# Kernel tuning notes

Hardware: AMD Instinct MI355X
Metric: run time of the kernel (lower is better)

The kernel has to match this reference:

```python
import jax, jax.numpy as jnp
import numpy as np

K_NEIGHBORS = 3  # init kwarg k_neighbors


def setup_inputs() -> dict:
    key = jax.random.key(0)
    k1, k2 = jax.random.split(key)
    q = jax.random.normal(k1, (75, 640, 21, 21), dtype=jnp.float32)
    S = jax.random.normal(k2, (5, 640, 21, 21), dtype=jnp.float32)
    return {"q": q, "S": S, "qAV_num": 1, "SAV_num": 1, "shot_num": 1}


def reference(q, S, qAV_num, SAV_num, shot_num):
    B, C = q.shape[0], q.shape[1]
    # [B, HW, C], L2-normalize each local descriptor over channels
    qd = q.reshape(B, C, -1).transpose(0, 2, 1)
    qd = qd / jnp.linalg.norm(qd, axis=2, keepdims=True)

    N = S.shape[0]
    sd = S.reshape(N, C, -1).transpose(0, 2, 1)  # [N, HW, C]
    sd = sd / jnp.linalg.norm(sd, axis=2, keepdims=True)
    HW = sd.shape[1]
    M = SAV_num * shot_num * HW
    # group support images into classes: [ncls, C, M]
    sup = sd.reshape(-1, M, C).transpose(0, 2, 1)
    ncls = sup.shape[0]

    # cosine similarity: [B, ncls, HW, M]
    ip = jnp.einsum('bqc,ncm->bnqm', qd, sup)
    # split AV groups: [B//qAV, qAV, ncls, HW, M]
    ip = ip.reshape(B // qAV_num, qAV_num, ncls, HW, M)
    # top-k along the query-descriptor (HW) axis (torch dim=-2)
    topk = jax.lax.top_k(jnp.swapaxes(ip, -1, -2), K_NEIGHBORS)[0]  # [..., M, k]
    img2class = topk.sum(axis=(-1, -2))  # [B', qAV, ncls]
    # geometric mean over the AV axis (dim=1)
    sim = jnp.exp(jnp.mean(jnp.log(img2class), axis=1))  # [B', ncls]
    return sim
```

## Files before the change

### kernel.cpp

```cpp
#include <hip/hip_runtime.h>
#include <hip/hip_bf16.h>


#define B_IMGS 75
#define N_CLS  5
#define C_DIM  640
#define HW     441
#define HWP    448
#define NKT    20
#define NRB    28
#define CHUNK  512

typedef __attribute__((ext_vector_type(8))) short  short8;
typedef __attribute__((ext_vector_type(4))) float  float4v;

__device__ __forceinline__ void ins3(float& t0, float& t1, float& t2, float v) {
    float m  = fminf(t0, v);
    t0 = fmaxf(t0, v);
    float m2 = fminf(t1, m);
    t1 = fmaxf(t1, m);
    t2 = fmaxf(t2, m2);
}

__device__ __forceinline__ void glds16(const __hip_bfloat16* g, __hip_bfloat16* l) {
    __builtin_amdgcn_global_load_lds(
        (const __attribute__((address_space(1))) unsigned int*)g,
        (__attribute__((address_space(3))) unsigned int*)l, 16, 0, 0);
}

__global__ __launch_bounds__(256)
void prep_kernel(const float* __restrict__ q, const float* __restrict__ S,
                 __hip_bfloat16* __restrict__ qn2, __hip_bfloat16* __restrict__ sn2) {
    __shared__ __hip_bfloat16 tile[C_DIM][65];
    __shared__ float part[4][64];
    __shared__ float inv[64];

    int bid = blockIdx.x;
    int img = bid / 7;
    int h0  = bid % 7;
    const float* src; __hip_bfloat16* dst;
    if (img < B_IMGS) {
        src = q + (size_t)img * C_DIM * HW;
        dst = qn2 + (size_t)img * NRB * NKT * CHUNK;
    } else {
        src = S + (size_t)(img - B_IMGS) * C_DIM * HW;
        dst = sn2 + (size_t)(img - B_IMGS) * NRB * NKT * CHUNK;
    }
    int t  = threadIdx.x;
    int hl = t & 63;
    int p  = t >> 6;
    int hw = h0 * 64 + hl;
    bool ok = hw < HW;
    int hwc = ok ? hw : (HW - 1);

    float ss = 0.f;
#pragma unroll 16
    for (int c = p * 160; c < (p + 1) * 160; ++c) {
        float v = src[(size_t)c * HW + hwc];
        ss += v * v;
    }
    part[p][hl] = ss;
    __syncthreads();
    if (t < 64) {
        float tot = part[0][t] + part[1][t] + part[2][t] + part[3][t];
        bool okr = (h0 * 64 + t) < HW;
        inv[t] = okr ? rsqrtf(tot) : 0.f;
    }
    __syncthreads();

    float iv = inv[hl];
#pragma unroll 8
    for (int c = p * 160; c < (p + 1) * 160; ++c) {
        float v = src[(size_t)c * HW + hwc] * iv;
        tile[c][hl] = __float2bfloat16(v);
    }
    __syncthreads();

    int rl  = t >> 2;
    int k8  = (t & 3) * 8;
    int rb  = h0 * 4 + (rl >> 4);
    int r16 = rl & 15;
    for (int kt = 0; kt < NKT; ++kt) {
        short8 v;
#pragma unroll
        for (int j = 0; j < 8; ++j) {
            __hip_bfloat16 h = tile[kt * 32 + k8 + j][rl];
            v[j] = *(short*)&h;
        }
        *(short8*)(dst + ((size_t)rb * NKT + kt) * CHUNK + r16 * 32 + k8) = v;
    }
}

__global__ __launch_bounds__(256, 2)
void gemm_top3_kernel(const __hip_bfloat16* __restrict__ qn2,
                      const __hip_bfloat16* __restrict__ sn2,
                      float* __restrict__ out) {
    __shared__ __hip_bfloat16 sbuf[64 * CHUNK];
    __shared__ float mrg[4][64][3];

    int id  = blockIdx.x;
    int xcd = id & 7;
    int j8  = id >> 3;
    int b   = (j8 / 35) * 8 + xcd;
    if (b >= B_IMGS) return;
    int inner = j8 % 35;
    int n  = inner / 7;
    int mt = inner % 7;

    int tid  = threadIdx.x;
    int w    = tid >> 6;
    int lane = tid & 63;
    int c16  = lane & 15;
    int quad = lane >> 4;
    int frag = c16 * 32 + quad * 8;

    const __hip_bfloat16* qA = qn2 + (size_t)b * NRB * NKT * CHUNK;
    const __hip_bfloat16* qB = sn2 + ((size_t)n * NRB + mt * 4) * NKT * CHUNK;

    float4v acc[7][4];
#pragma unroll
    for (int r = 0; r < 7; ++r)
#pragma unroll
        for (int j = 0; j < 4; ++j)
            acc[r][j] = (float4v){0.f, 0.f, 0.f, 0.f};

    for (int s = 0; s < 10; ++s) {
        __syncthreads();
#pragma unroll
        for (int i = 0; i < 16; ++i) {
            int cid = w * 16 + i;
            const __hip_bfloat16* g;
            if (cid < 56) {
                int rb = cid >> 1;
                g = qA + ((size_t)rb * NKT + 2 * s + (cid & 1)) * CHUNK;
            } else {
                int jb = (cid - 56) >> 1;
                g = qB + ((size_t)jb * NKT + 2 * s + (cid & 1)) * CHUNK;
            }
            glds16(g + lane * 8, sbuf + cid * CHUNK + lane * 8);
        }
        __syncthreads();

#pragma unroll
        for (int kk = 0; kk < 2; ++kk) {
            short8 a[7], bfr[4];
#pragma unroll
            for (int r = 0; r < 7; ++r)
                a[r] = *(const short8*)(sbuf + ((r * 4 + w) * 2 + kk) * CHUNK + frag);
#pragma unroll
            for (int j = 0; j < 4; ++j)
                bfr[j] = *(const short8*)(sbuf + (56 + j * 2 + kk) * CHUNK + frag);
#pragma unroll
            for (int r = 0; r < 7; ++r)
#pragma unroll
                for (int j = 0; j < 4; ++j)
                    acc[r][j] = __builtin_amdgcn_mfma_f32_16x16x32_bf16(
                        a[r], bfr[j], acc[r][j], 0, 0, 0);
        }
    }

    float T0[4], T1[4], T2[4];
#pragma unroll
    for (int j = 0; j < 4; ++j) { T0[j] = -1e30f; T1[j] = -1e30f; T2[j] = -1e30f; }
#pragma unroll
    for (int r = 0; r < 7; ++r)
#pragma unroll
        for (int j = 0; j < 4; ++j)
#pragma unroll
            for (int g = 0; g < 4; ++g) {
                int row = r * 64 + w * 16 + quad * 4 + g;
                float v = (row < HW) ? acc[r][j][g] : -1e30f;
                ins3(T0[j], T1[j], T2[j], v);
            }

#pragma unroll
    for (int j = 0; j < 4; ++j) {
#pragma unroll
        for (int d = 16; d <= 32; d <<= 1) {
            float o0 = __shfl_xor(T0[j], d, 64);
            float o1 = __shfl_xor(T1[j], d, 64);
            float o2 = __shfl_xor(T2[j], d, 64);
            ins3(T0[j], T1[j], T2[j], o0);
            ins3(T0[j], T1[j], T2[j], o1);
            ins3(T0[j], T1[j], T2[j], o2);
        }
    }

    if (quad == 0) {
#pragma unroll
        for (int j = 0; j < 4; ++j) {
            mrg[w][j * 16 + c16][0] = T0[j];
            mrg[w][j * 16 + c16][1] = T1[j];
            mrg[w][j * 16 + c16][2] = T2[j];
        }
    }
    __syncthreads();
    if (tid < 64) {
        int col = tid;
        float t0 = mrg[0][col][0], t1 = mrg[0][col][1], t2 = mrg[0][col][2];
#pragma unroll
        for (int ww = 1; ww < 4; ++ww) {
            ins3(t0, t1, t2, mrg[ww][col][0]);
            ins3(t0, t1, t2, mrg[ww][col][1]);
            ins3(t0, t1, t2, mrg[ww][col][2]);
        }
        float s = (mt * 64 + col < HW) ? (t0 + t1 + t2) : 0.f;
#pragma unroll
        for (int d = 32; d >= 1; d >>= 1) s += __shfl_xor(s, d, 64);
        if (tid == 0) atomicAdd(&out[b * N_CLS + n], s);
    }
}

extern "C" void kernel_launch(void* const* d_in, const int* in_sizes, int n_in,
                              void* d_out, int out_size, void* d_ws, size_t ws_size,
                              hipStream_t stream) {
    const float* q = (const float*)d_in[0];
    const float* S = (const float*)d_in[1];
    float* out = (float*)d_out;

    char* ws = (char*)d_ws;
    size_t off = 0;
    __hip_bfloat16* qn2 = (__hip_bfloat16*)(ws + off);
    off += (size_t)B_IMGS * NRB * NKT * CHUNK * 2;  off = (off + 255) & ~(size_t)255;
    __hip_bfloat16* sn2 = (__hip_bfloat16*)(ws + off);

    hipMemsetAsync(d_out, 0, (size_t)out_size * sizeof(float), stream);

    prep_kernel<<<dim3(80 * 7), dim3(256), 0, stream>>>(q, S, qn2, sn2);
    gemm_top3_kernel<<<dim3(8 * 350), dim3(256), 0, stream>>>(qn2, sn2, out);
}
```

Measured before the change: 288.9 us.

## Split prep into norm and pack kernels with finer grid and new fragment layout

Splits the normalize-and-pack preprocessing into a norm kernel that writes inverse norms to workspace and a pack kernel launched with five times more blocks, each handling a 128-channel slice. The aim is more parallelism and far less shared memory per block in the pack stage, where the old single kernel held a 640x65 tile. The packed chunk layout changes so each lane's 8-element MFMA fragment sits contiguously at lane*8, and the GEMM's fragment index is updated to match. The cost is an extra launch, a second read of the input, and an inverse-norm buffer round trip.

```diff
diff --git a/kernel.cpp b/kernel.cpp
--- a/kernel.cpp
+++ b/kernel.cpp
@@ -10,6 +10,7 @@
 #define NKT    20
 #define NRB    28
 #define CHUNK  512
+#define TPAD   66
 
 typedef __attribute__((ext_vector_type(8))) short  short8;
 typedef __attribute__((ext_vector_type(4))) float  float4v;
@@ -29,15 +30,47 @@
 }
 
 __global__ __launch_bounds__(256)
-void prep_kernel(const float* __restrict__ q, const float* __restrict__ S,
-                 __hip_bfloat16* __restrict__ qn2, __hip_bfloat16* __restrict__ sn2) {
-    __shared__ __hip_bfloat16 tile[C_DIM][65];
+void norm_kernel(const float* __restrict__ q, const float* __restrict__ S,
+                 float* __restrict__ invn) {
     __shared__ float part[4][64];
-    __shared__ float inv[64];
-
     int bid = blockIdx.x;
     int img = bid / 7;
     int h0  = bid % 7;
+    const float* src = (img < B_IMGS)
+        ? q + (size_t)img * C_DIM * HW
+        : S + (size_t)(img - B_IMGS) * C_DIM * HW;
+    int t  = threadIdx.x;
+    int hl = t & 63;
+    int p  = t >> 6;
+    int hw = h0 * 64 + hl;
+    int hwc = (hw < HW) ? hw : (HW - 1);
+
+    float ss = 0.f;
+    for (int c0 = p * 160; c0 < (p + 1) * 160; c0 += 16) {
+        float v[16];
+#pragma unroll
+        for (int j = 0; j < 16; ++j) v[j] = src[(size_t)(c0 + j) * HW + hwc];
+#pragma unroll
+        for (int j = 0; j < 16; ++j) ss += v[j] * v[j];
+    }
+    part[p][hl] = ss;
+    __syncthreads();
+    if (t < 64) {
+        float tot = part[0][t] + part[1][t] + part[2][t] + part[3][t];
+        invn[img * HWP + h0 * 64 + t] = (h0 * 64 + t < HW) ? rsqrtf(tot) : 0.f;
+    }
+}
+
+__global__ __launch_bounds__(256)
+void pack_kernel(const float* __restrict__ q, const float* __restrict__ S,
+                 const float* __restrict__ invn,
+                 __hip_bfloat16* __restrict__ qn2, __hip_bfloat16* __restrict__ sn2) {
+    __shared__ __hip_bfloat16 tile[128][TPAD];
+    int bid = blockIdx.x;
+    int img = bid / 35;
+    int rem = bid % 35;
+    int h0  = rem / 5;
+    int ktg = rem % 5;
     const float* src; __hip_bfloat16* dst;
     if (img < B_IMGS) {
         src = q + (size_t)img * C_DIM * HW;
@@ -50,44 +83,33 @@
     int hl = t & 63;
     int p  = t >> 6;
     int hw = h0 * 64 + hl;
-    bool ok = hw < HW;
-    int hwc = ok ? hw : (HW - 1);
-
-    float ss = 0.f;
-#pragma unroll 16
-    for (int c = p * 160; c < (p + 1) * 160; ++c) {
-        float v = src[(size_t)c * HW + hwc];
-        ss += v * v;
-    }
-    part[p][hl] = ss;
+    int hwc = (hw < HW) ? hw : (HW - 1);
+    float iv = invn[img * HWP + h0 * 64 + hl];
+
+    for (int c0 = p * 32; c0 < p * 32 + 32; c0 += 8) {
+        float v[8];
+#pragma unroll
+        for (int j = 0; j < 8; ++j)
+            v[j] = src[(size_t)(ktg * 128 + c0 + j) * HW + hwc];
+#pragma unroll
+        for (int j = 0; j < 8; ++j)
+            tile[c0 + j][hl] = __float2bfloat16(v[j] * iv);
+    }
     __syncthreads();
-    if (t < 64) {
-        float tot = part[0][t] + part[1][t] + part[2][t] + part[3][t];
-        bool okr = (h0 * 64 + t) < HW;
-        inv[t] = okr ? rsqrtf(tot) : 0.f;
-    }
-    __syncthreads();
-
-    float iv = inv[hl];
-#pragma unroll 8
-    for (int c = p * 160; c < (p + 1) * 160; ++c) {
-        float v = src[(size_t)c * HW + hwc] * iv;
-        tile[c][hl] = __float2bfloat16(v);
-    }
-    __syncthreads();
-
-    int rl  = t >> 2;
-    int k8  = (t & 3) * 8;
-    int rb  = h0 * 4 + (rl >> 4);
-    int r16 = rl & 15;
-    for (int kt = 0; kt < NKT; ++kt) {
+
+    int tl  = t & 63;
+    int row = tl & 15;
+    int oct = tl >> 4;
+    int rb  = h0 * 4 + p;
+    for (int ktl = 0; ktl < 4; ++ktl) {
+        int kt = ktg * 4 + ktl;
         short8 v;
 #pragma unroll
         for (int j = 0; j < 8; ++j) {
-            __hip_bfloat16 h = tile[kt * 32 + k8 + j][rl];
-            v[j] = *(short*)&h;
-        }
-        *(short8*)(dst + ((size_t)rb * NKT + kt) * CHUNK + r16 * 32 + k8) = v;
+            __hip_bfloat16 hv = tile[ktl * 32 + oct * 8 + j][p * 16 + row];
+            v[j] = *(short*)&hv;
+        }
+        *(short8*)(dst + ((size_t)rb * NKT + kt) * CHUNK + tl * 8) = v;
     }
 }
 
@@ -112,7 +134,7 @@
     int lane = tid & 63;
     int c16  = lane & 15;
     int quad = lane >> 4;
-    int frag = c16 * 32 + quad * 8;
+    int frag = lane * 8;
 
     const __hip_bfloat16* qA = qn2 + (size_t)b * NRB * NKT * CHUNK;
     const __hip_bfloat16* qB = sn2 + ((size_t)n * NRB + mt * 4) * NKT * CHUNK;
@@ -223,9 +245,12 @@
     __hip_bfloat16* qn2 = (__hip_bfloat16*)(ws + off);
     off += (size_t)B_IMGS * NRB * NKT * CHUNK * 2;  off = (off + 255) & ~(size_t)255;
     __hip_bfloat16* sn2 = (__hip_bfloat16*)(ws + off);
+    off += (size_t)N_CLS * NRB * NKT * CHUNK * 2;   off = (off + 255) & ~(size_t)255;
+    float* invn = (float*)(ws + off);
 
     hipMemsetAsync(d_out, 0, (size_t)out_size * sizeof(float), stream);
 
-    prep_kernel<<<dim3(80 * 7), dim3(256), 0, stream>>>(q, S, qn2, sn2);
+    norm_kernel<<<dim3(80 * 7), dim3(256), 0, stream>>>(q, S, invn);
+    pack_kernel<<<dim3(80 * 7 * 5), dim3(256), 0, stream>>>(q, S, invn, qn2, sn2);
     gemm_top3_kernel<<<dim3(8 * 350), dim3(256), 0, stream>>>(qn2, sn2, out);
 }
```

After: 284.0 us. About the same (-1.7%).
